# Kernel optimization log

Hardware: AMD Instinct MI355X
Metric: run time of the kernel (lower is better)

Reference implementation:

```python
import jax, jax.numpy as jnp
import numpy as np

HID = 3584   # hidden_size
NH = 28      # num_attention_heads
NKV = 4      # num_key_value_heads
HD = 128     # head_dim
S = 4        # packed samples
L = 1024     # tokens per sample (sample_lens = [L]*S)
T = S * L
THETA = 1000000.0
EPS = 1e-6


def rmsnorm(x, w):
    # Qwen2NavitRMSNorm (fp32 math)
    v = jnp.mean(x * x, axis=-1, keepdims=True)
    return w * (x * jax.lax.rsqrt(v + EPS))


def rotate_half(x):
    d = x.shape[-1] // 2
    return jnp.concatenate([-x[..., d:], x[..., :d]], axis=-1)


def setup_inputs() -> dict:
    key = jax.random.key(0)
    ks = jax.random.split(key, 12)
    sc = 0.02
    x = jax.random.normal(ks[0], (T, HID), jnp.float32)
    # rotary embeddings: positions restart per packed sample
    pos = jnp.tile(jnp.arange(L, dtype=jnp.float32), S)
    inv = 1.0 / (THETA ** (jnp.arange(0, HD, 2, dtype=jnp.float32) / HD))
    fr = pos[:, None] * inv[None, :]
    emb = jnp.concatenate([fr, fr], axis=-1)  # [T, HD]
    und_idx = jnp.arange(0, T, 2, dtype=jnp.int32)  # interleaved und/gen tokens
    gen_idx = jnp.arange(1, T, 2, dtype=jnp.int32)
    n = lambda k, shp: jax.random.normal(k, shp, jnp.float32) * sc
    return dict(
        packed_sequence=x, cos=jnp.cos(emb), sin=jnp.sin(emb),
        wq=n(ks[1], (NH * HD, HID)), bq=jnp.zeros((NH * HD,), jnp.float32),
        wk=n(ks[2], (NKV * HD, HID)), bk=jnp.zeros((NKV * HD,), jnp.float32),
        wv=n(ks[3], (NKV * HD, HID)), bv=jnp.zeros((NKV * HD,), jnp.float32),
        wo=n(ks[4], (HID, NH * HD)),
        wqg=n(ks[5], (NH * HD, HID)), bqg=jnp.zeros((NH * HD,), jnp.float32),
        wkg=n(ks[6], (NKV * HD, HID)), bkg=jnp.zeros((NKV * HD,), jnp.float32),
        wvg=n(ks[7], (NKV * HD, HID)), bvg=jnp.zeros((NKV * HD,), jnp.float32),
        wog=n(ks[8], (HID, NH * HD)),
        qn=jnp.ones((HD,), jnp.float32), kn=jnp.ones((HD,), jnp.float32),
        qng=jnp.ones((HD,), jnp.float32), kng=jnp.ones((HD,), jnp.float32),
        und_idx=und_idx, gen_idx=gen_idx,
    )


def reference(packed_sequence, cos, sin, wq, bq, wk, bk, wv, bv, wo,
              wqg, bqg, wkg, bkg, wvg, bvg, wog, qn, kn, qng, kng,
              und_idx, gen_idx):
    x = packed_sequence
    xu = x[und_idx]
    xg = x[gen_idx]

    def dual_proj(wu, bu, wg, bg, dim):
        out = jnp.zeros((T, dim), x.dtype)
        out = out.at[und_idx].set(xu @ wu.T + bu)
        out = out.at[gen_idx].set(xg @ wg.T + bg)
        return out

    q = dual_proj(wq, bq, wqg, bqg, NH * HD).reshape(T, NH, HD)
    k = dual_proj(wk, bk, wkg, bkg, NKV * HD).reshape(T, NKV, HD)
    v = dual_proj(wv, bv, wvg, bvg, NKV * HD).reshape(T, NKV, HD)

    # per-modality qk RMSNorm
    q = jnp.zeros_like(q).at[und_idx].set(rmsnorm(q[und_idx], qn)).at[gen_idx].set(rmsnorm(q[gen_idx], qng))
    k = jnp.zeros_like(k).at[und_idx].set(rmsnorm(k[und_idx], kn)).at[gen_idx].set(rmsnorm(k[gen_idx], kng))

    # RoPE (unsqueeze_dim=1 -> broadcast over heads)
    c = cos[:, None, :]
    s = sin[:, None, :]
    q = q * c + rotate_half(q) * s
    k = k * c + rotate_half(k) * s

    # GQA expand kv heads (consecutive repeat matches repeat+reshape in torch)
    grp = NH // NKV
    k = jnp.repeat(k, grp, axis=1)  # [T, NH, HD]
    v = jnp.repeat(v, grp, axis=1)

    # packed -> per-sample causal attention (all sample_lens equal)
    qh = q.reshape(S, L, NH, HD)
    kh = k.reshape(S, L, NH, HD)
    vh = v.reshape(S, L, NH, HD)
    scores = jnp.einsum('slhd,smhd->shlm', qh, kh) / np.float32(np.sqrt(HD))
    causal = jnp.tril(jnp.ones((L, L), bool))
    scores = jnp.where(causal, scores, jnp.float32(-1e30))
    p = jax.nn.softmax(scores, axis=-1)
    attn = jnp.einsum('shlm,smhd->slhd', p, vh).reshape(T, NH * HD)

    out = jnp.zeros((T, HID), x.dtype)
    out = out.at[und_idx].set(attn[und_idx] @ wo.T)
    out = out.at[gen_idx].set(attn[gen_idx] @ wog.T)
    return out
```

## Files before the change

### kernel.cpp

```cpp
#include <hip/hip_runtime.h>
#include <hip/hip_bf16.h>

#define T_TOK 4096
#define HID   3584
#define NH    28
#define NKV   4
#define HD    128
#define SEG   4
#define LSEQ  1024
#define KDIM  3584
#define BKG   64

typedef __attribute__((ext_vector_type(8))) short bf16x8;
typedef __attribute__((ext_vector_type(4))) float f32x4;

#define GLOAD16(g, l) __builtin_amdgcn_global_load_lds( \
    (const __attribute__((address_space(1))) void*)(g), \
    (__attribute__((address_space(3))) void*)(l), 16, 0, 0)

__device__ __forceinline__ unsigned short f2bf(float f) {
    unsigned u = __float_as_uint(f);
    return (unsigned short)((u + 0x7fffu + ((u >> 16) & 1u)) >> 16);
}
__device__ __forceinline__ float bf2f(unsigned short u) {
    return __uint_as_float(((unsigned)u) << 16);
}

__device__ __forceinline__ f32x4 mfma16(bf16x8 a, bf16x8 b, f32x4 c) {
    return __builtin_amdgcn_mfma_f32_16x16x32_bf16(a, b, c, 0, 0, 0);
}


__global__ void cvt4_f32_bf16(const float* __restrict__ s0, const float* __restrict__ s1,
                              const float* __restrict__ s2, const float* __restrict__ s3,
                              unsigned short* __restrict__ d0, unsigned short* __restrict__ d1,
                              unsigned short* __restrict__ d2, unsigned short* __restrict__ d3,
                              int n4) {
    const float* s; unsigned short* d;
    switch (blockIdx.y) {
        case 0: s = s0; d = d0; break;
        case 1: s = s1; d = d1; break;
        case 2: s = s2; d = d2; break;
        default: s = s3; d = d3; break;
    }
    int i = blockIdx.x * 256 + threadIdx.x;
    if (i >= n4) return;
    float4 v = reinterpret_cast<const float4*>(s)[i];
    ushort4 o;
    o.x = f2bf(v.x); o.y = f2bf(v.y); o.z = f2bf(v.z); o.w = f2bf(v.w);
    reinterpret_cast<ushort4*>(d)[i] = o;
}

__global__ void cvt_x_split(const float* __restrict__ x,
                            unsigned short* __restrict__ xu, unsigned short* __restrict__ xg) {
    int i = blockIdx.x * 256 + threadIdx.x;
    int t = i / (HID / 4);
    int c = i - t * (HID / 4);
    float4 v = reinterpret_cast<const float4*>(x)[i];
    ushort4 o;
    o.x = f2bf(v.x); o.y = f2bf(v.y); o.z = f2bf(v.z); o.w = f2bf(v.w);
    unsigned short* dst = ((t & 1) ? xg : xu) + (size_t)(t >> 1) * HID + c * 4;
    *reinterpret_cast<ushort4*>(dst) = o;
}

__device__ __forceinline__ void gemm256_core(const unsigned short* __restrict__ Aptr,
                                             const unsigned short* __restrict__ Bptr,
                                             unsigned short* ldsbase, f32x4 (&acc)[8][4],
                                             int kb, int kend) {
    const int tid = threadIdx.x;
    const int lane = tid & 63, w = tid >> 6;
    const int wr = w >> 2, wc = w & 3;
    const int lr = lane & 15, lkg = lane >> 4;
    char* const L = (char*)ldsbase;

    int src_off[4];
#pragma unroll
    for (int j = 0; j < 4; j++) {
        int r = j * 64 + (tid >> 3);
        int clog = (tid & 7) ^ ((tid >> 3) & 7);
        src_off[j] = r * KDIM + clog * 8;
    }
    const int aoff0 = (wr * 128 + lr) * 128 + ((lkg ^ (lr & 7)) << 4);
    const int boff0 = (wc * 64 + lr) * 128 + ((lkg ^ (lr & 7)) << 4) + 32768;

    bf16x8 a[4][2], b[4][2];
#pragma unroll
    for (int m = 0; m < 8; m++)
#pragma unroll
        for (int n = 0; n < 4; n++) acc[m][n] = (f32x4){0.f, 0.f, 0.f, 0.f};

#define STG_A(buf, k0, h) do { _Pragma("unroll") for (int jj = 0; jj < 2; jj++) { \
    int j = (h) * 2 + jj; \
    GLOAD16(Aptr + src_off[j] + (k0), L + (buf) * 65536 + j * 8192 + tid * 16); } } while (0)
#define STG_B(buf, k0, h) do { _Pragma("unroll") for (int jj = 0; jj < 2; jj++) { \
    int j = (h) * 2 + jj; \
    GLOAD16(Bptr + src_off[j] + (k0), L + (buf) * 65536 + 32768 + j * 8192 + tid * 16); } } while (0)
#define RD_A(buf, mh) do { _Pragma("unroll") for (int mm = 0; mm < 4; mm++) { \
    int ro = (buf) * 65536 + aoff0 + ((mh) * 4 + mm) * 2048; \
    a[mm][0] = *(const bf16x8*)(L + ro); \
    a[mm][1] = *(const bf16x8*)(L + (ro ^ 64)); } } while (0)
#define RD_B(buf, nh) do { _Pragma("unroll") for (int nn = 0; nn < 2; nn++) { \
    int ro = (buf) * 65536 + boff0 + ((nh) * 2 + nn) * 2048; \
    b[(nh) * 2 + nn][0] = *(const bf16x8*)(L + ro); \
    b[(nh) * 2 + nn][1] = *(const bf16x8*)(L + (ro ^ 64)); } } while (0)
#define MM(mh, nh) do { _Pragma("unroll") for (int mm = 0; mm < 4; mm++) \
    _Pragma("unroll") for (int nn = 0; nn < 2; nn++) \
    _Pragma("unroll") for (int ks = 0; ks < 2; ks++) \
        acc[(mh) * 4 + mm][(nh) * 2 + nn] = \
            mfma16(a[mm][ks], b[(nh) * 2 + nn][ks], acc[(mh) * 4 + mm][(nh) * 2 + nn]); } while (0)
#define BAR   asm volatile("s_barrier" ::: "memory")
#define LGKM0 do { asm volatile("s_waitcnt lgkmcnt(0)" ::: "memory"); \
                   __builtin_amdgcn_sched_barrier(0); } while (0)
#define VMC4  asm volatile("s_waitcnt vmcnt(4)" ::: "memory")
#define PHI   __builtin_amdgcn_s_setprio(1)
#define PLO   __builtin_amdgcn_s_setprio(0)

    STG_A(0, kb, 0); STG_A(0, kb, 1); STG_B(0, kb, 0); STG_B(0, kb, 1);
    STG_B(1, kb + BKG, 0); STG_B(1, kb + BKG, 1);
    VMC4;
    BAR;

    const int iters = (kend - kb) / (2 * BKG);
#pragma unroll 1
    for (int t = 0; t < iters; ++t) {
        int k1 = kb + (2 * t + 1) * BKG;
        int k2 = kb + (2 * t + 2) * BKG; if (k2 > kend - BKG) k2 = kend - BKG;
        int k3 = kb + (2 * t + 3) * BKG; if (k3 > kend - BKG) k3 = kend - BKG;
        RD_A(0, 0); RD_B(0, 0); STG_A(1, k1, 0);
        BAR; LGKM0; PHI; MM(0, 0); PLO; BAR;
        RD_B(0, 1); STG_A(1, k1, 1);
        BAR; LGKM0; PHI; MM(0, 1); PLO; BAR;
        RD_A(0, 1); STG_B(0, k2, 0);
        BAR; LGKM0; PHI; MM(1, 0); PLO; BAR;
        STG_B(0, k2, 1);
        BAR; LGKM0; PHI; MM(1, 1); PLO; VMC4; BAR;
        RD_A(1, 0); RD_B(1, 0); STG_A(0, k2, 0);
        BAR; LGKM0; PHI; MM(0, 0); PLO; BAR;
        RD_B(1, 1); STG_A(0, k2, 1);
        BAR; LGKM0; PHI; MM(0, 1); PLO; BAR;
        RD_A(1, 1); STG_B(1, k3, 0);
        BAR; LGKM0; PHI; MM(1, 0); PLO; BAR;
        STG_B(1, k3, 1);
        BAR; LGKM0; PHI; MM(1, 1); PLO; VMC4; BAR;
    }
    asm volatile("s_waitcnt vmcnt(0)" ::: "memory");

#undef STG_A
#undef STG_B
#undef RD_A
#undef RD_B
#undef MM
#undef BAR
#undef LGKM0
#undef VMC4
#undef PHI
#undef PLO
}

__global__ __launch_bounds__(512, 2) void qkv_gemm8(
    const unsigned short* __restrict__ xu, const unsigned short* __restrict__ xg,
    const unsigned short* __restrict__ wq0, const unsigned short* __restrict__ wk0,
    const unsigned short* __restrict__ wv0, const unsigned short* __restrict__ wq1,
    const unsigned short* __restrict__ wk1, const unsigned short* __restrict__ wv1,
    const float* __restrict__ bq0, const float* __restrict__ bk0, const float* __restrict__ bv0,
    const float* __restrict__ bq1, const float* __restrict__ bk1, const float* __restrict__ bv1,
    unsigned short* __restrict__ qp, unsigned short* __restrict__ kp,
    unsigned short* __restrict__ vp) {
    __shared__ unsigned short lds[65536];
    const int bid = blockIdx.x;
    int nb, ks, bm, kb, klen;
    if (bid < 448) {
        nb = bid >> 5;
        int rem = bid & 31;
        ks = rem >> 4; bm = rem & 15;
        kb = ks * 1792; klen = 1792;
    } else {
        int e = bid - 448;
        int g = e >> 6;
        int rem = e & 63;
        ks = rem >> 4; bm = rem & 15;
        nb = 14 + g;
        kb = ks * 896; klen = 896;
    }
    const int par = bm >> 3, mb = bm & 7;
    const unsigned short* A = (par ? xg : xu) + (size_t)mb * 256 * KDIM;
    const unsigned short* W;
    const float* bias;
    unsigned short* C;
    int ldc, col0;
    if (nb < 14) {
        W = (par ? wq1 : wq0) + (size_t)nb * 256 * KDIM;
        bias = (par ? bq1 : bq0); C = qp; ldc = NH * HD; col0 = nb * 256;
    } else if (nb < 16) {
        W = (par ? wk1 : wk0) + (size_t)(nb - 14) * 256 * KDIM;
        bias = (par ? bk1 : bk0); C = kp; ldc = NKV * HD; col0 = (nb - 14) * 256;
    } else {
        W = (par ? wv1 : wv0) + (size_t)(nb - 16) * 256 * KDIM;
        bias = (par ? bv1 : bv0); C = vp; ldc = NKV * HD; col0 = (nb - 16) * 256;
    }
    C += (size_t)ks * T_TOK * ldc;
    f32x4 acc[8][4];
    gemm256_core(A, W, lds, acc, kb, kb + klen);

    const int lane = threadIdx.x & 63, w = threadIdx.x >> 6;
    const int wr = w >> 2, wc = w & 3, lr = lane & 15, lkg = lane >> 4;
#pragma unroll
    for (int n = 0; n < 4; n++) {
        int colt = col0 + wc * 64 + n * 16 + lr;
        float bb = (ks == 0) ? bias[colt] : 0.f;
#pragma unroll
        for (int m = 0; m < 8; m++) {
#pragma unroll
            for (int rg = 0; rg < 4; rg++) {
                int tr = mb * 256 + wr * 128 + m * 16 + lkg * 4 + rg;
                int tok = 2 * tr + par;
                C[(size_t)tok * ldc + colt] = f2bf(acc[m][n][rg] + bb);
            }
        }
    }
}

__global__ __launch_bounds__(512, 2) void oproj_gemm8(
    const unsigned short* __restrict__ au, const unsigned short* __restrict__ ag,
    const unsigned short* __restrict__ wo0, const unsigned short* __restrict__ wo1,
    float* __restrict__ out) {
    __shared__ unsigned short lds[65536];
    const int bid = blockIdx.x;
    const int bm = bid & 15, nb = bid >> 4;
    const int par = bm >> 3, mb = bm & 7;
    const unsigned short* A = (par ? ag : au) + (size_t)mb * 256 * KDIM;
    const unsigned short* W = (par ? wo1 : wo0) + (size_t)nb * 256 * KDIM;
    f32x4 acc[8][4];
    gemm256_core(A, W, lds, acc, 0, KDIM);

    const int lane = threadIdx.x & 63, w = threadIdx.x >> 6;
    const int wr = w >> 2, wc = w & 3, lr = lane & 15, lkg = lane >> 4;
#pragma unroll
    for (int n = 0; n < 4; n++) {
        int col = nb * 256 + wc * 64 + n * 16 + lr;
#pragma unroll
        for (int m = 0; m < 8; m++) {
#pragma unroll
            for (int rg = 0; rg < 4; rg++) {
                int tr = mb * 256 + wr * 128 + m * 16 + lkg * 4 + rg;
                int tok = 2 * tr + par;
                out[(size_t)tok * HID + col] = acc[m][n][rg];
            }
        }
    }
}

__global__ void normrope2(const unsigned short* __restrict__ qp, const unsigned short* __restrict__ kp,
                          const float* __restrict__ cosb, const float* __restrict__ sinb,
                          const float* __restrict__ qn, const float* __restrict__ kn,
                          const float* __restrict__ qng, const float* __restrict__ kng,
                          unsigned short* __restrict__ q_bf, unsigned short* __restrict__ k_bf) {
    const int t = blockIdx.x, w = threadIdx.x >> 6, lane = threadIdx.x & 63;
    const int h = blockIdx.y * 4 + w;
    const bool isq = (h < 28);
    float v0, v1;
    if (isq) {
        const unsigned short* src = qp + (size_t)t * (NH * HD) + h * HD;
        const size_t S = (size_t)T_TOK * NH * HD;
        v0 = bf2f(src[lane]) + bf2f(src[S + lane]);
        v1 = bf2f(src[lane + 64]) + bf2f(src[S + lane + 64]);
    } else {
        const unsigned short* src = kp + (size_t)t * (NKV * HD) + (h - 28) * HD;
        const size_t S = (size_t)T_TOK * NKV * HD;
        v0 = bf2f(src[lane]) + bf2f(src[S + lane]) + bf2f(src[2 * S + lane]) + bf2f(src[3 * S + lane]);
        v1 = bf2f(src[lane + 64]) + bf2f(src[S + lane + 64]) +
             bf2f(src[2 * S + lane + 64]) + bf2f(src[3 * S + lane + 64]);
    }
    float ss = v0 * v0 + v1 * v1;
#pragma unroll
    for (int off = 32; off >= 1; off >>= 1) ss += __shfl_xor(ss, off, 64);
    float inv = rsqrtf(ss * (1.f / 128.f) + 1e-6f);
    const float* wn = isq ? ((t & 1) ? qng : qn) : ((t & 1) ? kng : kn);
    float n0 = v0 * inv * wn[lane], n1 = v1 * inv * wn[lane + 64];
    float c0 = cosb[(size_t)t * HD + lane], c1 = cosb[(size_t)t * HD + lane + 64];
    float s0 = sinb[(size_t)t * HD + lane], s1 = sinb[(size_t)t * HD + lane + 64];
    float o0 = n0 * c0 - n1 * s0;
    float o1 = n1 * c1 + n0 * s1;
    unsigned short* dst = isq ? q_bf + (size_t)t * (NH * HD) + h * HD
                              : k_bf + (size_t)t * (NKV * HD) + (h - 28) * HD;
    dst[lane] = f2bf(o0);
    dst[lane + 64] = f2bf(o1);
}

__global__ void vtrans(const unsigned short* __restrict__ vp, unsigned short* __restrict__ vT) {
    const int lb = blockIdx.x, sh = blockIdx.y;
    const int s = sh >> 2, hv = sh & 3, d = threadIdx.x;
    const size_t S = (size_t)T_TOK * NKV * HD;
    unsigned short tmp[8];
#pragma unroll
    for (int i = 0; i < 8; i++) {
        size_t idx = ((size_t)(s * LSEQ + lb * 8 + i)) * (NKV * HD) + hv * HD + d;
        tmp[i] = f2bf(bf2f(vp[idx]) + bf2f(vp[S + idx]) + bf2f(vp[2 * S + idx]) + bf2f(vp[3 * S + idx]));
    }
    *(bf16x8*)(vT + ((size_t)sh * HD + d) * LSEQ + lb * 8) = *(bf16x8*)tmp;
}

__global__ __launch_bounds__(512, 4) void attn_fwd(
    const unsigned short* __restrict__ q_bf, const unsigned short* __restrict__ k_bf,
    const unsigned short* __restrict__ vT,
    unsigned short* __restrict__ au, unsigned short* __restrict__ ag) {
    __shared__ unsigned short kt[2][64 * 128];
    __shared__ unsigned short vt[2][128 * 64];
    __shared__ unsigned short pt[8][16 * 64];

    const int qbk = 7 - blockIdx.x;
    const int h = blockIdx.y, s = blockIdx.z;
    const int hk = h / 7;
    const int tid = threadIdx.x, lane = tid & 63, w = tid >> 6;
    const int lr = lane & 15, lkg = lane >> 4;
    const int qg = qbk * 128 + w * 16 + lr;

    bf16x8 qf[4];
    {
        const unsigned short* qp =
            q_bf + ((size_t)(s * LSEQ + qg)) * (NH * HD) + h * HD;
#pragma unroll
        for (int kk = 0; kk < 4; kk++) qf[kk] = *(const bf16x8*)(qp + kk * 32 + lkg * 8);
    }
    asm volatile("s_waitcnt vmcnt(0)" ::: "memory");

    float m_r = -1e30f, l_r = 0.f;
    f32x4 accO[8];
#pragma unroll
    for (int dn = 0; dn < 8; dn++) accO[dn] = (f32x4){0.f, 0.f, 0.f, 0.f};

    const float scale = 0.08838834764831843f;
    const int nkt = 2 * qbk + 2;

#define STAGE_KV(buf, ktile) do { _Pragma("unroll") for (int i = 0; i < 2; i++) { \
    int o = i * 8192 + tid * 16; \
    { int r = o >> 8; int sc = ((o >> 4) & 15) ^ (r & 7); \
      GLOAD16(k_bf + ((size_t)(s * LSEQ + (ktile) * 64 + r)) * (NKV * HD) + hk * HD + sc * 8, \
              (char*)kt[buf] + o); } \
    { int r = o >> 7; int sc = ((o >> 4) & 7) ^ (r & 7); \
      GLOAD16(vT + ((size_t)((s * NKV + hk) * HD + r)) * LSEQ + (ktile) * 64 + sc * 8, \
              (char*)vt[buf] + o); } } } while (0)

    STAGE_KV(0, 0);

#pragma unroll 1
    for (int ktile = 0; ktile < nkt; ++ktile) {
        const int cur = ktile & 1;
        if (ktile + 1 < nkt) {
            STAGE_KV(cur ^ 1, ktile + 1);
            asm volatile("s_waitcnt vmcnt(4)" ::: "memory");
        } else {
            asm volatile("s_waitcnt vmcnt(0)" ::: "memory");
        }
        asm volatile("s_barrier" ::: "memory");

        f32x4 accT[4];
#pragma unroll
        for (int n = 0; n < 4; n++) accT[n] = (f32x4){0.f, 0.f, 0.f, 0.f};
#pragma unroll
        for (int n = 0; n < 4; n++) {
            int r = n * 16 + lr;
#pragma unroll
            for (int kk = 0; kk < 4; kk++) {
                bf16x8 kf = *(const bf16x8*)((const char*)kt[cur] + r * 256 +
                                             (((kk * 4 + lkg) ^ (r & 7)) << 4));
                accT[n] = mfma16(kf, qf[kk], accT[n]);
            }
        }
        float mnew = -1e30f;
#pragma unroll
        for (int n = 0; n < 4; n++) {
#pragma unroll
            for (int rg = 0; rg < 4; rg++) {
                int kvg = ktile * 64 + n * 16 + lkg * 4 + rg;
                float sv = accT[n][rg] * scale;
                sv = (kvg <= qg) ? sv : -1e30f;
                accT[n][rg] = sv;
                mnew = fmaxf(mnew, sv);
            }
        }
        mnew = fmaxf(mnew, __shfl_xor(mnew, 16, 64));
        mnew = fmaxf(mnew, __shfl_xor(mnew, 32, 64));
        if (__any(mnew > m_r + 8.f)) {
            float mc = fmaxf(m_r, mnew);
            float alpha = __expf(m_r - mc);
            m_r = mc;
            l_r *= alpha;
            float ab[4];
#pragma unroll
            for (int rg = 0; rg < 4; rg++) ab[rg] = __shfl(alpha, lkg * 4 + rg, 64);
#pragma unroll
            for (int dn = 0; dn < 8; dn++)
#pragma unroll
                for (int rg = 0; rg < 4; rg++) accO[dn][rg] *= ab[rg];
        }
        float ls = 0.f;
#pragma unroll
        for (int n = 0; n < 4; n++) {
            unsigned short p4[4];
#pragma unroll
            for (int rg = 0; rg < 4; rg++) {
                float p = __expf(accT[n][rg] - m_r);
                ls += p;
                p4[rg] = f2bf(p);
            }
            int byte = lr * 128 + ((((n * 2 + (lkg >> 1)) ^ (lr & 7))) << 4) + (lkg & 1) * 8;
            *(uint2*)((char*)pt[w] + byte) = *(uint2*)p4;
        }
        ls += __shfl_xor(ls, 16, 64);
        ls += __shfl_xor(ls, 32, 64);
        l_r += ls;
#pragma unroll
        for (int kk2 = 0; kk2 < 2; kk2++) {
            bf16x8 pf = *(const bf16x8*)((const char*)pt[w] + lr * 128 +
                                         (((kk2 * 4 + lkg) ^ (lr & 7)) << 4));
#pragma unroll
            for (int dn = 0; dn < 8; dn++) {
                int r2 = dn * 16 + lr;
                bf16x8 vf = *(const bf16x8*)((const char*)vt[cur] + r2 * 128 +
                                             (((kk2 * 4 + lkg) ^ (r2 & 7)) << 4));
                accO[dn] = mfma16(pf, vf, accO[dn]);
            }
        }
        asm volatile("s_barrier" ::: "memory");
    }
#undef STAGE_KV

    float lb[4];
#pragma unroll
    for (int rg = 0; rg < 4; rg++) lb[rg] = __shfl(l_r, lkg * 4 + rg, 64);
#pragma unroll
    for (int dn = 0; dn < 8; dn++) {
#pragma unroll
        for (int rg = 0; rg < 4; rg++) {
            int row = qbk * 128 + w * 16 + lkg * 4 + rg;
            int t = s * LSEQ + row;
            unsigned short* dst = ((t & 1) ? ag : au) + (size_t)(t >> 1) * (NH * HD) +
                                  h * HD + dn * 16 + lr;
            *dst = f2bf(accO[dn][rg] / lb[rg]);
        }
    }
}

extern "C" void kernel_launch(void* const* d_in, const int* in_sizes, int n_in,
                              void* d_out, int out_size, void* d_ws, size_t ws_size,
                              hipStream_t stream) {
    const float* x    = (const float*)d_in[0];
    const float* cosb = (const float*)d_in[1];
    const float* sinb = (const float*)d_in[2];
    const float* wq   = (const float*)d_in[3];
    const float* bq   = (const float*)d_in[4];
    const float* wk   = (const float*)d_in[5];
    const float* bk   = (const float*)d_in[6];
    const float* wv   = (const float*)d_in[7];
    const float* bv   = (const float*)d_in[8];
    const float* wo   = (const float*)d_in[9];
    const float* wqg  = (const float*)d_in[10];
    const float* bqg  = (const float*)d_in[11];
    const float* wkg  = (const float*)d_in[12];
    const float* bkg  = (const float*)d_in[13];
    const float* wvg  = (const float*)d_in[14];
    const float* bvg  = (const float*)d_in[15];
    const float* wog  = (const float*)d_in[16];
    const float* qn   = (const float*)d_in[17];
    const float* kn   = (const float*)d_in[18];
    const float* qng  = (const float*)d_in[19];
    const float* kng  = (const float*)d_in[20];
    float* out = (float*)d_out;

    char* ws = (char*)d_ws;
    size_t off = 0;
    auto alloc = [&](size_t bytes) -> char* {
        char* p = ws + off;
        off += (bytes + 255) & ~(size_t)255;
        return p;
    };
    const size_t WQ_E = (size_t)3584 * 3584;
    const size_t WK_E = (size_t)512 * 3584;
    unsigned short* wqb  = (unsigned short*)alloc(WQ_E * 2);
    unsigned short* wqgb = (unsigned short*)alloc(WQ_E * 2);
    unsigned short* wob  = (unsigned short*)alloc(WQ_E * 2);
    unsigned short* wogb = (unsigned short*)alloc(WQ_E * 2);
    unsigned short* wkb  = (unsigned short*)alloc(WK_E * 2);
    unsigned short* wkgb = (unsigned short*)alloc(WK_E * 2);
    unsigned short* wvb  = (unsigned short*)alloc(WK_E * 2);
    unsigned short* wvgb = (unsigned short*)alloc(WK_E * 2);
    unsigned short* xu   = (unsigned short*)alloc((size_t)2048 * HID * 2);
    unsigned short* xg   = (unsigned short*)alloc((size_t)2048 * HID * 2);
    unsigned short* qp = (unsigned short*)alloc((size_t)2 * T_TOK * (NH * HD) * 2);
    unsigned short* kp = (unsigned short*)alloc((size_t)4 * T_TOK * (NKV * HD) * 2);
    unsigned short* vp = (unsigned short*)alloc((size_t)4 * T_TOK * (NKV * HD) * 2);
    unsigned short* q_bf = wqb;
    unsigned short* k_bf = wqb + (size_t)T_TOK * (NH * HD);
    unsigned short* vTb  = k_bf + (size_t)T_TOK * (NKV * HD);
    unsigned short* au = qp;
    unsigned short* ag = au + (size_t)2048 * (NH * HD);

    if (ws_size < off) return;

    cvt_x_split<<<T_TOK * (HID / 4) / 256, 256, 0, stream>>>(x, xu, xg);
    cvt4_f32_bf16<<<dim3((int)(WQ_E / 4 / 256), 4), 256, 0, stream>>>(
        wq, wqg, wo, wog, wqb, wqgb, wob, wogb, (int)(WQ_E / 4));
    cvt4_f32_bf16<<<dim3((int)(WK_E / 4 / 256), 4), 256, 0, stream>>>(
        wk, wkg, wv, wvg, wkb, wkgb, wvb, wvgb, (int)(WK_E / 4));

    qkv_gemm8<<<dim3(704), 512, 0, stream>>>(xu, xg, wqb, wkb, wvb, wqgb, wkgb, wvgb,
                                             bq, bk, bv, bqg, bkg, bvg, qp, kp, vp);
    normrope2<<<dim3(T_TOK, 8), 256, 0, stream>>>(qp, kp, cosb, sinb,
                                                  qn, kn, qng, kng, q_bf, k_bf);
    vtrans<<<dim3(128, 16), 128, 0, stream>>>(vp, vTb);
    attn_fwd<<<dim3(8, NH, SEG), 512, 0, stream>>>(q_bf, k_bf, vTb, au, ag);
    oproj_gemm8<<<dim3(224), 512, 0, stream>>>(au, ag, wob, wogb, out);
}
```

Before: 462.8 us.

## Overlap wo conversion with attention, fuse V transpose into norm-rope, remap oproj blocks

The fp32-to-bf16 conversion of the output projection weights moves out of the upfront conversion kernel and into 128 extra blocks of the attention launch, so it runs alongside attention work. The V reduce-and-transpose kernel is folded into normrope2 as an extra grid row, which removes one launch. The oproj block index mapping is reordered for different cache locality across weight tiles. The risk is that conversion blocks compete with attention blocks for compute units, and the attention grid is flattened into a 1D index.

```diff
diff --git a/kernel.cpp b/kernel.cpp
--- a/kernel.cpp
+++ b/kernel.cpp
@@ -10,6 +10,7 @@
 #define LSEQ  1024
 #define KDIM  3584
 #define BKG   64
+#define NCVT  128
 
 typedef __attribute__((ext_vector_type(8))) short bf16x8;
 typedef __attribute__((ext_vector_type(4))) float f32x4;
@@ -226,7 +227,8 @@
     float* __restrict__ out) {
     __shared__ unsigned short lds[65536];
     const int bid = blockIdx.x;
-    const int bm = bid & 15, nb = bid >> 4;
+    const int x = bid & 7, i = bid >> 3;
+    const int nb = i >> 1, bm = x * 2 + (i & 1);
     const int par = bm >> 3, mb = bm & 7;
     const unsigned short* A = (par ? ag : au) + (size_t)mb * 256 * KDIM;
     const unsigned short* W = (par ? wo1 : wo0) + (size_t)nb * 256 * KDIM;
@@ -251,10 +253,29 @@
 }
 
 __global__ void normrope2(const unsigned short* __restrict__ qp, const unsigned short* __restrict__ kp,
+                          const unsigned short* __restrict__ vp,
                           const float* __restrict__ cosb, const float* __restrict__ sinb,
                           const float* __restrict__ qn, const float* __restrict__ kn,
                           const float* __restrict__ qng, const float* __restrict__ kng,
-                          unsigned short* __restrict__ q_bf, unsigned short* __restrict__ k_bf) {
+                          unsigned short* __restrict__ q_bf, unsigned short* __restrict__ k_bf,
+                          unsigned short* __restrict__ vT) {
+    if (blockIdx.y == 8) {
+        if (blockIdx.x >= 1024) return;
+        const int u = blockIdx.x * 2 + (threadIdx.x >> 7);
+        const int d = threadIdx.x & 127;
+        const int sh = u >> 7, lb = u & 127;
+        const int s = sh >> 2, hv = sh & 3;
+        const size_t S = (size_t)T_TOK * NKV * HD;
+        unsigned short tmp[8];
+#pragma unroll
+        for (int i = 0; i < 8; i++) {
+            size_t idx = ((size_t)(s * LSEQ + lb * 8 + i)) * (NKV * HD) + hv * HD + d;
+            tmp[i] = f2bf(bf2f(vp[idx]) + bf2f(vp[S + idx]) +
+                          bf2f(vp[2 * S + idx]) + bf2f(vp[3 * S + idx]));
+        }
+        *(bf16x8*)(vT + ((size_t)sh * HD + d) * LSEQ + lb * 8) = *(bf16x8*)tmp;
+        return;
+    }
     const int t = blockIdx.x, w = threadIdx.x >> 6, lane = threadIdx.x & 63;
     const int h = blockIdx.y * 4 + w;
     const bool isq = (h < 28);
@@ -287,31 +308,37 @@
     dst[lane + 64] = f2bf(o1);
 }
 
-__global__ void vtrans(const unsigned short* __restrict__ vp, unsigned short* __restrict__ vT) {
-    const int lb = blockIdx.x, sh = blockIdx.y;
-    const int s = sh >> 2, hv = sh & 3, d = threadIdx.x;
-    const size_t S = (size_t)T_TOK * NKV * HD;
-    unsigned short tmp[8];
-#pragma unroll
-    for (int i = 0; i < 8; i++) {
-        size_t idx = ((size_t)(s * LSEQ + lb * 8 + i)) * (NKV * HD) + hv * HD + d;
-        tmp[i] = f2bf(bf2f(vp[idx]) + bf2f(vp[S + idx]) + bf2f(vp[2 * S + idx]) + bf2f(vp[3 * S + idx]));
-    }
-    *(bf16x8*)(vT + ((size_t)sh * HD + d) * LSEQ + lb * 8) = *(bf16x8*)tmp;
-}
-
 __global__ __launch_bounds__(512, 4) void attn_fwd(
     const unsigned short* __restrict__ q_bf, const unsigned short* __restrict__ k_bf,
     const unsigned short* __restrict__ vT,
-    unsigned short* __restrict__ au, unsigned short* __restrict__ ag) {
+    unsigned short* __restrict__ au, unsigned short* __restrict__ ag,
+    const float* __restrict__ wof, const float* __restrict__ wogf,
+    unsigned short* __restrict__ wob, unsigned short* __restrict__ wogb) {
     __shared__ unsigned short kt[2][64 * 128];
     __shared__ unsigned short vt[2][128 * 64];
     __shared__ unsigned short pt[8][16 * 64];
 
-    const int qbk = 7 - blockIdx.x;
-    const int h = blockIdx.y, s = blockIdx.z;
+    const int bid = blockIdx.x;
+    const int tid = threadIdx.x;
+    if (bid < NCVT) {
+        const size_t n4 = (size_t)KDIM * KDIM / 4;
+        for (size_t i = (size_t)bid * 512 + tid; i < 2 * n4; i += (size_t)NCVT * 512) {
+            const float* sp = (i < n4) ? wof : wogf;
+            unsigned short* dp = (i < n4) ? wob : wogb;
+            size_t j = (i < n4) ? i : i - n4;
+            float4 v = reinterpret_cast<const float4*>(sp)[j];
+            ushort4 o;
+            o.x = f2bf(v.x); o.y = f2bf(v.y); o.z = f2bf(v.z); o.w = f2bf(v.w);
+            reinterpret_cast<ushort4*>(dp)[j] = o;
+        }
+        return;
+    }
+    const int e = bid - NCVT;
+    const int qbk = 7 - (e / 112);
+    const int rem = e % 112;
+    const int h = rem >> 2, s = rem & 3;
     const int hk = h / 7;
-    const int tid = threadIdx.x, lane = tid & 63, w = tid >> 6;
+    const int lane = tid & 63, w = tid >> 6;
     const int lr = lane & 15, lkg = lane >> 4;
     const int qg = qbk * 128 + w * 16 + lr;
 
@@ -426,9 +453,9 @@
     }
 #undef STAGE_KV
 
-    float lb[4];
-#pragma unroll
-    for (int rg = 0; rg < 4; rg++) lb[rg] = __shfl(l_r, lkg * 4 + rg, 64);
+    float lb4[4];
+#pragma unroll
+    for (int rg = 0; rg < 4; rg++) lb4[rg] = __shfl(l_r, lkg * 4 + rg, 64);
 #pragma unroll
     for (int dn = 0; dn < 8; dn++) {
 #pragma unroll
@@ -437,7 +464,7 @@
             int t = s * LSEQ + row;
             unsigned short* dst = ((t & 1) ? ag : au) + (size_t)(t >> 1) * (NH * HD) +
                                   h * HD + dn * 16 + lr;
-            *dst = f2bf(accO[dn][rg] / lb[rg]);
+            *dst = f2bf(accO[dn][rg] / lb4[rg]);
         }
     }
 }
@@ -499,16 +526,16 @@
     if (ws_size < off) return;
 
     cvt_x_split<<<T_TOK * (HID / 4) / 256, 256, 0, stream>>>(x, xu, xg);
-    cvt4_f32_bf16<<<dim3((int)(WQ_E / 4 / 256), 4), 256, 0, stream>>>(
-        wq, wqg, wo, wog, wqb, wqgb, wob, wogb, (int)(WQ_E / 4));
+    cvt4_f32_bf16<<<dim3((int)(WQ_E / 4 / 256), 2), 256, 0, stream>>>(
+        wq, wqg, wq, wqg, wqb, wqgb, wqb, wqgb, (int)(WQ_E / 4));
     cvt4_f32_bf16<<<dim3((int)(WK_E / 4 / 256), 4), 256, 0, stream>>>(
         wk, wkg, wv, wvg, wkb, wkgb, wvb, wvgb, (int)(WK_E / 4));
 
     qkv_gemm8<<<dim3(704), 512, 0, stream>>>(xu, xg, wqb, wkb, wvb, wqgb, wkgb, wvgb,
                                              bq, bk, bv, bqg, bkg, bvg, qp, kp, vp);
-    normrope2<<<dim3(T_TOK, 8), 256, 0, stream>>>(qp, kp, cosb, sinb,
-                                                  qn, kn, qng, kng, q_bf, k_bf);
-    vtrans<<<dim3(128, 16), 128, 0, stream>>>(vp, vTb);
-    attn_fwd<<<dim3(8, NH, SEG), 512, 0, stream>>>(q_bf, k_bf, vTb, au, ag);
+    normrope2<<<dim3(T_TOK, 9), 256, 0, stream>>>(qp, kp, vp, cosb, sinb,
+                                                  qn, kn, qng, kng, q_bf, k_bf, vTb);
+    attn_fwd<<<dim3(NCVT + 896), 512, 0, stream>>>(q_bf, k_bf, vTb, au, ag,
+                                                   wo, wog, wob, wogb);
     oproj_gemm8<<<dim3(224), 512, 0, stream>>>(au, ag, wob, wogb, out);
 }
```

Result: faster. 408.4 us (-11.8%).
